# Performance work log

Measured on AMD Instinct MI355X. Metric: run time of the kernel, lower is better.

Reference implementation:

```python
import jax, jax.numpy as jnp
import numpy as np

B, C, H, W = 8, 256, 48, 48
EPS = 1e-5


def setup_inputs() -> dict:
    key = jax.random.key(0)
    ks = jax.random.split(key, 14)
    n = lambda k, shape, s=1.0: jax.random.normal(k, shape, dtype=jnp.float32) * s
    return {
        "fea_left": n(ks[0], (B, C, H, W)),
        "fea_right": n(ks[1], (B, C, H, W)),
        # query branch: conv1x1 weight (out,in), bias, BN gamma/beta/running_mean/running_var
        "Wq": n(ks[2], (C, C), 0.05), "bq": n(ks[3], (C,), 0.05),
        "gq": 1.0 + n(ks[4], (C,), 0.05), "betaq": n(ks[5], (C,), 0.05),
        "mq": n(ks[6], (C,), 0.05),
        "vq": jax.random.uniform(ks[7], (C,), dtype=jnp.float32, minval=0.5, maxval=1.5),
        # key branch
        "Wk": n(ks[8], (C, C), 0.05), "bk": n(ks[9], (C,), 0.05),
        "gk": 1.0 + n(ks[10], (C,), 0.05), "betak": n(ks[11], (C,), 0.05),
        "mk": n(ks[12], (C,), 0.05),
        "vk": jax.random.uniform(ks[13], (C,), dtype=jnp.float32, minval=0.5, maxval=1.5),
    }


def _proj(x, Wt, b, g, beta, m, v):
    # conv1x1 (bias=True) followed by eval-mode BatchNorm2d
    y = jnp.einsum("bchw,oc->bohw", x, Wt) + b[:, None, None]
    scale = g * jax.lax.rsqrt(v + EPS)
    return (y - m[:, None, None]) * scale[:, None, None] + beta[:, None, None]


def reference(fea_left, fea_right, Wq, bq, gq, betaq, mq, vq, Wk, bk, gk, betak, mk, vk):
    b, c, h, w = fea_left.shape

    def attend(qsrc, ksrc, vsrc):
        # torch .view(b,-1,c): raw row-major reinterpretation -> plain reshape
        Q = _proj(qsrc, Wq, bq, gq, betaq, mq, vq).reshape(b, -1, c)  # (b, h*w, c)
        K = _proj(ksrc, Wk, bk, gk, betak, mk, vk).reshape(b, -1, c)
        A = jax.nn.softmax(jnp.einsum("bnc,bmc->bnm", Q, K) / c, axis=-1)
        out = jnp.einsum("bnm,bmc->bnc", A, vsrc.reshape(b, -1, c))
        return out.transpose(0, 2, 1).reshape(b, c, h, w)

    cxr = attend(fea_left, fea_right, fea_right)
    enh = attend(fea_right, fea_left, fea_left)
    return (cxr, enh)
```

## Files before the change

kernel.cpp:

```cpp
#include <hip/hip_runtime.h>

#define CH    256
#define NTOK  2304
#define MATSZ (CH * NTOK)

typedef __bf16 bf16x8 __attribute__((ext_vector_type(8)));
typedef float  f4v    __attribute__((ext_vector_type(4)));
typedef float  f16v   __attribute__((ext_vector_type(16)));
typedef unsigned int u32x4 __attribute__((ext_vector_type(4)));

__device__ __forceinline__ unsigned short f2bf(float f) {
    union { float f; unsigned int i; } c;
    c.f = f;
    unsigned int x = c.i;
    x += 0x7fffu + ((x >> 16) & 1u);
    return (unsigned short)(x >> 16);
}

__device__ __forceinline__ bf16x8 cvt8(const float* p) {
    union { bf16x8 v; unsigned short s[8]; } u;
#pragma unroll
    for (int i = 0; i < 8; ++i) u.s[i] = f2bf(p[i]);
    return u.v;
}

__global__ __launch_bounds__(256) void tpose_k(
    const float* __restrict__ inL,
    const float* __restrict__ inR,
    unsigned short* __restrict__ out, int R, int Ccols)
{
    __shared__ unsigned short tile[64][72];
    int mat = blockIdx.y;
    const float* in = (mat >= 8 ? inR : inL) + (size_t)(mat & 7) * MATSZ;
    unsigned short* o = out + (size_t)mat * MATSZ;
    int tC = Ccols >> 6;
    int r0 = (blockIdx.x / tC) << 6;
    int c0 = (blockIdx.x % tC) << 6;
    int t = threadIdx.x;
    int col = t & 63, rs = t >> 6;
#pragma unroll
    for (int i = 0; i < 16; ++i) {
        int row = rs + i * 4;
        tile[row][col] = f2bf(in[(size_t)(r0 + row) * Ccols + c0 + col]);
    }
    __syncthreads();
#pragma unroll
    for (int i = 0; i < 16; ++i) {
        int crow = rs + i * 4;
        o[(size_t)(c0 + crow) * R + r0 + col] = tile[col][crow];
    }
}

__global__ __launch_bounds__(256, 2) void proj_k(
    const unsigned short* __restrict__ XT,
    const float* __restrict__ Wq_, const float* __restrict__ Wk_,
    const float* __restrict__ bq_, const float* __restrict__ bk_,
    const float* __restrict__ gq_, const float* __restrict__ gk_,
    const float* __restrict__ beq_, const float* __restrict__ bek_,
    const float* __restrict__ mq_, const float* __restrict__ mk_,
    const float* __restrict__ vq_, const float* __restrict__ vk_,
    unsigned short* __restrict__ Yout)
{
    __shared__ __align__(16) unsigned short Xs[64][264];
    int pb = blockIdx.y;
    int p = pb >> 3, b = pb & 7;
    int s = p & 1, br = p >> 1;
    const unsigned short* X = XT + (size_t)(s * 8 + b) * MATSZ;
    const float* W  = br ? Wk_ : Wq_;
    const float* bb = br ? bk_ : bq_;
    const float* gg = br ? gk_ : gq_;
    const float* be = br ? bek_ : beq_;
    const float* mm = br ? mk_ : mq_;
    const float* vv = br ? vk_ : vq_;
    unsigned short* Yo = Yout + (size_t)pb * MATSZ;

    int ot = blockIdx.x & 3, pt = blockIdx.x >> 2;
    int o0 = ot * 64, pos0 = pt * 64;
    int t = threadIdx.x;
    int w = t >> 6, lane = t & 63;
    int l15 = lane & 15, quad = lane >> 4;

    {
        int r = t >> 2, cq = (t & 3) << 6;
        const unsigned short* src = X + (size_t)(pos0 + r) * CH + cq;
        unsigned short* dst = &Xs[r][cq];
#pragma unroll
        for (int k = 0; k < 8; ++k)
            *(u32x4*)(dst + k * 8) = *(const u32x4*)(src + k * 8);
    }
    bf16x8 wf[8];
    {
        const float* wp = W + (size_t)(o0 + w * 16 + l15) * CH + quad * 8;
#pragma unroll
        for (int kc = 0; kc < 8; ++kc)
            wf[kc] = cvt8(wp + kc * 32);
    }
    __syncthreads();

    f4v zero4 = {0.f, 0.f, 0.f, 0.f};
    f4v acc[4] = {zero4, zero4, zero4, zero4};
#pragma unroll
    for (int kc = 0; kc < 8; ++kc) {
#pragma unroll
        for (int ct = 0; ct < 4; ++ct) {
            bf16x8 xb = *(const bf16x8*)(&Xs[ct * 16 + l15][kc * 32 + quad * 8]);
            acc[ct] = __builtin_amdgcn_mfma_f32_16x16x32_bf16(wf[kc], xb, acc[ct], 0, 0, 0);
        }
    }
#pragma unroll
    for (int r = 0; r < 4; ++r) {
        int o = o0 + w * 16 + quad * 4 + r;
        float scale = gg[o] * rsqrtf(vv[o] + 1e-5f);
        float shift = (bb[o] - mm[o]) * scale + be[o];
#pragma unroll
        for (int ct = 0; ct < 4; ++ct) {
            float val = acc[ct][r] * scale + shift;
            Yo[(size_t)o * NTOK + pos0 + ct * 16 + l15] = f2bf(val);
        }
    }
}

__global__ __launch_bounds__(256, 2) void attn_k(
    const unsigned short* __restrict__ Y,
    const unsigned short* __restrict__ VT,
    float* __restrict__ out)
{
    __shared__ __align__(16) unsigned char lds[74240];
    unsigned char* Ks = lds;
    unsigned char* Vs = lds + 32768;
    unsigned char* Pb = lds + 65536;
    float*         Ls = (float*)(lds + 73728);

    int bid = blockIdx.x;
    int wg = (bid & 7) * 72 + (bid >> 3);
    int qt = wg % 36;
    int ab = wg / 36;
    int a = ab >> 3, b = ab & 7;
    const unsigned short* Qp = Y + (size_t)(a * 8 + b) * MATSZ;
    const unsigned short* Kp = Y + (size_t)((3 - a) * 8 + b) * MATSZ;
    const unsigned short* Vp = VT + (size_t)((1 - a) * 8 + b) * MATSZ;
    float* Op = out + (size_t)ab * MATSZ;

    int t = threadIdx.x;
    int w = t >> 6, lane = t & 63;
    int l31 = lane & 31, h = lane >> 5;
    int qb = w >> 1;
    int kb = w & 1;
    int chh = w & 1;
    int rxor = (l31 & 7) << 4;

    const unsigned char* kS = (const unsigned char*)Kp
        + ((t * 16) ^ (((t >> 5) & 7) << 4));
    const unsigned char* vS = (const unsigned char*)Vp
        + (size_t)(t >> 3) * 4608
        + (((t & 7) * 16) ^ (((t >> 3) & 7) << 4));
    unsigned char* kD = Ks + t * 16;
    unsigned char* vD = Vs + t * 16;

    bf16x8 qf[16];
    {
        const unsigned short* qp = Qp + (size_t)(qt * 64 + qb * 32 + l31) * CH + h * 8;
#pragma unroll
        for (int ks = 0; ks < 16; ++ks)
            qf[ks] = *(const bf16x8*)(qp + ks * 16);
    }

    f16v acc_o[4];
#pragma unroll
    for (int c = 0; c < 4; ++c)
#pragma unroll
        for (int r = 0; r < 16; ++r) acc_o[c][r] = 0.f;
    float l_acc[16];
#pragma unroll
    for (int r = 0; r < 16; ++r) l_acc[r] = 0.f;

    for (int kt = 0; kt < 36; ++kt) {
        __syncthreads();
#pragma unroll
        for (int k = 0; k < 8; ++k)
            __builtin_amdgcn_global_load_lds(
                (const unsigned int*)(kS + (size_t)kt * 32768 + k * 4096),
                (unsigned int*)(kD + k * 4096), 16, 0, 0);
#pragma unroll
        for (int k = 0; k < 8; ++k)
            __builtin_amdgcn_global_load_lds(
                (const unsigned int*)(vS + (size_t)kt * 128 + (size_t)k * 147456),
                (unsigned int*)(vD + k * 4096), 16, 0, 0);
        __syncthreads();

        f16v accs;
#pragma unroll
        for (int r = 0; r < 16; ++r) accs[r] = 0.f;
        const unsigned char* krow = Ks + ((kb * 32 + l31) << 9);
#pragma unroll
        for (int ks = 0; ks < 16; ++ks) {
            bf16x8 kf = *(const bf16x8*)(krow + ((ks * 32 + h * 16) ^ rxor));
            accs = __builtin_amdgcn_mfma_f32_32x32x16_bf16(qf[ks], kf, accs, 0, 0, 0);
        }
#pragma unroll
        for (int r = 0; r < 16; ++r) {
            float pe = __expf(accs[r] * (1.0f / 256.0f));
            l_acc[r] += pe;
            int row = (r & 3) + 8 * (r >> 2) + 4 * h;
            int q = qb * 32 + row;
            *(__bf16*)(Pb + q * 128 + ((kb * 64 + l31 * 2) ^ ((row & 7) << 4))) = (__bf16)pe;
        }
        __syncthreads();

#pragma unroll
        for (int ks2 = 0; ks2 < 4; ++ks2) {
            bf16x8 pf = *(const bf16x8*)(Pb + ((qb * 32 + l31) << 7)
                                       + ((ks2 * 32 + h * 16) ^ rxor));
#pragma unroll
            for (int chb = 0; chb < 4; ++chb) {
                int ch = chh * 128 + chb * 32 + l31;
                bf16x8 vf = *(const bf16x8*)(Vs + (ch << 7)
                                           + ((ks2 * 32 + h * 16) ^ rxor));
                acc_o[chb] = __builtin_amdgcn_mfma_f32_32x32x16_bf16(pf, vf, acc_o[chb], 0, 0, 0);
            }
        }
    }

#pragma unroll
    for (int r = 0; r < 16; ++r) {
        float rs = l_acc[r];
        rs += __shfl_xor(rs, 1, 64);
        rs += __shfl_xor(rs, 2, 64);
        rs += __shfl_xor(rs, 4, 64);
        rs += __shfl_xor(rs, 8, 64);
        rs += __shfl_xor(rs, 16, 64);
        l_acc[r] = rs;
    }
    if (l31 == 0) {
#pragma unroll
        for (int r = 0; r < 16; ++r) {
            int row = (r & 3) + 8 * (r >> 2) + 4 * h;
            Ls[w * 32 + row] = l_acc[r];
        }
    }
    __syncthreads();
    float l_tot[16];
#pragma unroll
    for (int r = 0; r < 16; ++r) {
        int row = (r & 3) + 8 * (r >> 2) + 4 * h;
        l_tot[r] = Ls[w * 32 + row] + Ls[(w ^ 1) * 32 + row];
    }

    float* Ot = (float*)lds;
#pragma unroll
    for (int chb = 0; chb < 4; ++chb) {
        int c = chh * 128 + chb * 32 + l31;
        int cx = (c & 7) << 2;
#pragma unroll
        for (int rr = 0; rr < 4; ++rr) {
            f4v v4;
#pragma unroll
            for (int i = 0; i < 4; ++i)
                v4[i] = acc_o[chb][rr * 4 + i] / l_tot[rr * 4 + i];
            int q0 = qb * 32 + rr * 8 + h * 4;
            *(f4v*)(Ot + c * 64 + (q0 ^ cx)) = v4;
        }
    }
    __syncthreads();
#pragma unroll
    for (int p = 0; p < 16; ++p) {
        int c = p * 16 + (t >> 4);
        int q = (t & 15) * 4;
        f4v v4 = *(const f4v*)(Ot + c * 64 + (q ^ ((c & 7) << 2)));
        *(f4v*)(Op + (size_t)c * NTOK + qt * 64 + q) = v4;
    }
}

extern "C" void kernel_launch(void* const* d_in, const int* in_sizes, int n_in,
                              void* d_out, int out_size, void* d_ws, size_t ws_size,
                              hipStream_t stream) {
    (void)in_sizes; (void)n_in; (void)out_size; (void)ws_size;
    const float* feaL  = (const float*)d_in[0];
    const float* feaR  = (const float*)d_in[1];
    const float* Wq    = (const float*)d_in[2];
    const float* bq    = (const float*)d_in[3];
    const float* gq    = (const float*)d_in[4];
    const float* betaq = (const float*)d_in[5];
    const float* mq    = (const float*)d_in[6];
    const float* vq    = (const float*)d_in[7];
    const float* Wk    = (const float*)d_in[8];
    const float* bk    = (const float*)d_in[9];
    const float* gk    = (const float*)d_in[10];
    const float* betak = (const float*)d_in[11];
    const float* mk    = (const float*)d_in[12];
    const float* vk    = (const float*)d_in[13];

    unsigned short* XT = (unsigned short*)d_ws;
    unsigned short* VT = XT;
    unsigned short* Yb = XT + (size_t)16 * MATSZ;
    float* out = (float*)d_out;

    dim3 blk(256);
    tpose_k<<<dim3(144, 16), blk, 0, stream>>>(feaL, feaR, XT, 256, 2304);
    proj_k<<<dim3(144, 32), blk, 0, stream>>>(XT, Wq, Wk, bq, bk, gq, gk,
                                              betaq, betak, mq, mk, vq, vk, Yb);
    tpose_k<<<dim3(144, 16), blk, 0, stream>>>(feaL, feaR, VT, 2304, 256);
    attn_k<<<dim3(576), blk, 0, stream>>>(Yb, VT, out);
}
```

Before: 340.2 us.

## Prefetch next K/V tile into registers instead of direct global-to-LDS loads

Replaces the synchronous global_load_lds copies of K and V tiles with register prefetching: the next tile is loaded into registers while the current tile is being computed, then written to swizzled LDS after the barrier. The goal is to hide global memory latency behind the MFMA and softmax work. The cost is 64 extra VGPRs per thread, which may reduce occupancy, and an extra register-to-LDS store step.

```diff
diff --git a/kernel.cpp b/kernel.cpp
--- a/kernel.cpp
+++ b/kernel.cpp
@@ -149,13 +149,10 @@
     int chh = w & 1;
     int rxor = (l31 & 7) << 4;
 
-    const unsigned char* kS = (const unsigned char*)Kp
-        + ((t * 16) ^ (((t >> 5) & 7) << 4));
-    const unsigned char* vS = (const unsigned char*)Vp
-        + (size_t)(t >> 3) * 4608
-        + (((t & 7) * 16) ^ (((t >> 3) & 7) << 4));
-    unsigned char* kD = Ks + t * 16;
-    unsigned char* vD = Vs + t * 16;
+    const unsigned short* ksrc0 = Kp + t * 8;
+    const unsigned short* vsrc0 = Vp + (size_t)(t >> 3) * NTOK + ((t & 7) << 3);
+    char* kdst = (char*)Ks + ((t * 16) ^ (((t >> 5) & 7) << 4));
+    char* vdst = (char*)Vs + ((t * 16) ^ (((t >> 3) & 7) << 4));
 
     bf16x8 qf[16];
     {
@@ -174,19 +171,28 @@
 #pragma unroll
     for (int r = 0; r < 16; ++r) l_acc[r] = 0.f;
 
+    u32x4 kreg[8], vreg[8];
+#pragma unroll
+    for (int k = 0; k < 8; ++k) kreg[k] = *(const u32x4*)(ksrc0 + k * 2048);
+#pragma unroll
+    for (int k = 0; k < 8; ++k) vreg[k] = *(const u32x4*)(vsrc0 + (size_t)k * 32 * NTOK);
+
     for (int kt = 0; kt < 36; ++kt) {
         __syncthreads();
 #pragma unroll
-        for (int k = 0; k < 8; ++k)
-            __builtin_amdgcn_global_load_lds(
-                (const unsigned int*)(kS + (size_t)kt * 32768 + k * 4096),
-                (unsigned int*)(kD + k * 4096), 16, 0, 0);
-#pragma unroll
-        for (int k = 0; k < 8; ++k)
-            __builtin_amdgcn_global_load_lds(
-                (const unsigned int*)(vS + (size_t)kt * 128 + (size_t)k * 147456),
-                (unsigned int*)(vD + k * 4096), 16, 0, 0);
+        for (int k = 0; k < 8; ++k) *(u32x4*)(kdst + k * 4096) = kreg[k];
+#pragma unroll
+        for (int k = 0; k < 8; ++k) *(u32x4*)(vdst + k * 4096) = vreg[k];
         __syncthreads();
+
+        if (kt < 35) {
+            const unsigned short* kn = ksrc0 + (size_t)(kt + 1) * 16384;
+            const unsigned short* vn = vsrc0 + (size_t)(kt + 1) * 64;
+#pragma unroll
+            for (int k = 0; k < 8; ++k) kreg[k] = *(const u32x4*)(kn + k * 2048);
+#pragma unroll
+            for (int k = 0; k < 8; ++k) vreg[k] = *(const u32x4*)(vn + (size_t)k * 32 * NTOK);
+        }
 
         f16v accs;
 #pragma unroll
```

After: 411.1 us. 1.21x slower.

## Double-buffer K tiles in LDS and stream V directly into registers

Applied to the files above, without the earlier changes.

The attention loop now prefetches the next K tile into a second LDS buffer, reusing the region that used to hold V. V fragments are loaded straight from global memory into registers at the top of each iteration instead of being staged through LDS. The full __syncthreads calls are replaced with explicit s_waitcnt plus s_barrier so the in-flight prefetch does not block progress. Launch bounds are relaxed to one block per SM to leave room for the extra V registers. The trade-offs are redundant V global reads across waves, global-load latency exposed inside each iteration, and possibly lower occupancy.

```diff
diff --git a/kernel.cpp b/kernel.cpp
--- a/kernel.cpp
+++ b/kernel.cpp
@@ -120,14 +120,13 @@
     }
 }
 
-__global__ __launch_bounds__(256, 2) void attn_k(
+__global__ __launch_bounds__(256, 1) void attn_k(
     const unsigned short* __restrict__ Y,
     const unsigned short* __restrict__ VT,
     float* __restrict__ out)
 {
     __shared__ __align__(16) unsigned char lds[74240];
     unsigned char* Ks = lds;
-    unsigned char* Vs = lds + 32768;
     unsigned char* Pb = lds + 65536;
     float*         Ls = (float*)(lds + 73728);
 
@@ -151,11 +150,8 @@
 
     const unsigned char* kS = (const unsigned char*)Kp
         + ((t * 16) ^ (((t >> 5) & 7) << 4));
-    const unsigned char* vS = (const unsigned char*)Vp
-        + (size_t)(t >> 3) * 4608
-        + (((t & 7) * 16) ^ (((t >> 3) & 7) << 4));
     unsigned char* kD = Ks + t * 16;
-    unsigned char* vD = Vs + t * 16;
+    const unsigned short* VpT = Vp + (size_t)(chh * 128 + l31) * NTOK + h * 8;
 
     bf16x8 qf[16];
     {
@@ -174,24 +170,40 @@
 #pragma unroll
     for (int r = 0; r < 16; ++r) l_acc[r] = 0.f;
 
+#pragma unroll
+    for (int k = 0; k < 8; ++k)
+        __builtin_amdgcn_global_load_lds(
+            (const unsigned int*)(kS + k * 4096),
+            (unsigned int*)(kD + k * 4096), 16, 0, 0);
+
     for (int kt = 0; kt < 36; ++kt) {
-        __syncthreads();
-#pragma unroll
-        for (int k = 0; k < 8; ++k)
-            __builtin_amdgcn_global_load_lds(
-                (const unsigned int*)(kS + (size_t)kt * 32768 + k * 4096),
-                (unsigned int*)(kD + k * 4096), 16, 0, 0);
-#pragma unroll
-        for (int k = 0; k < 8; ++k)
-            __builtin_amdgcn_global_load_lds(
-                (const unsigned int*)(vS + (size_t)kt * 128 + (size_t)k * 147456),
-                (unsigned int*)(vD + k * 4096), 16, 0, 0);
-        __syncthreads();
+        bf16x8 vf[4][4];
+        {
+            const unsigned short* vp = VpT + kt * 64;
+#pragma unroll
+            for (int chb = 0; chb < 4; ++chb)
+#pragma unroll
+                for (int ks2 = 0; ks2 < 4; ++ks2)
+                    vf[chb][ks2] = *(const bf16x8*)(vp + (size_t)chb * 32 * NTOK + ks2 * 16);
+        }
+        {
+            int nt = kt + 1; if (nt == 36) nt = 0;
+            const unsigned char* ks_src = kS + (size_t)nt * 32768;
+            unsigned char* ks_dst = kD + ((kt + 1) & 1) * 32768;
+#pragma unroll
+            for (int k = 0; k < 8; ++k)
+                __builtin_amdgcn_global_load_lds(
+                    (const unsigned int*)(ks_src + k * 4096),
+                    (unsigned int*)(ks_dst + k * 4096), 16, 0, 0);
+        }
+        asm volatile("s_waitcnt vmcnt(24)" ::: "memory");
+        __builtin_amdgcn_s_barrier();
+        asm volatile("" ::: "memory");
 
         f16v accs;
 #pragma unroll
         for (int r = 0; r < 16; ++r) accs[r] = 0.f;
-        const unsigned char* krow = Ks + ((kb * 32 + l31) << 9);
+        const unsigned char* krow = Ks + (kt & 1) * 32768 + ((kb * 32 + l31) << 9);
 #pragma unroll
         for (int ks = 0; ks < 16; ++ks) {
             bf16x8 kf = *(const bf16x8*)(krow + ((ks * 32 + h * 16) ^ rxor));
@@ -205,19 +217,17 @@
             int q = qb * 32 + row;
             *(__bf16*)(Pb + q * 128 + ((kb * 64 + l31 * 2) ^ ((row & 7) << 4))) = (__bf16)pe;
         }
-        __syncthreads();
+        asm volatile("s_waitcnt lgkmcnt(0)" ::: "memory");
+        __builtin_amdgcn_s_barrier();
+        asm volatile("" ::: "memory");
 
 #pragma unroll
         for (int ks2 = 0; ks2 < 4; ++ks2) {
             bf16x8 pf = *(const bf16x8*)(Pb + ((qb * 32 + l31) << 7)
                                        + ((ks2 * 32 + h * 16) ^ rxor));
 #pragma unroll
-            for (int chb = 0; chb < 4; ++chb) {
-                int ch = chh * 128 + chb * 32 + l31;
-                bf16x8 vf = *(const bf16x8*)(Vs + (ch << 7)
-                                           + ((ks2 * 32 + h * 16) ^ rxor));
-                acc_o[chb] = __builtin_amdgcn_mfma_f32_32x32x16_bf16(pf, vf, acc_o[chb], 0, 0, 0);
-            }
+            for (int chb = 0; chb < 4; ++chb)
+                acc_o[chb] = __builtin_amdgcn_mfma_f32_32x32x16_bf16(pf, vf[chb][ks2], acc_o[chb], 0, 0, 0);
         }
     }
 
```

Measured after the change: 564.2 us. 1.66x slower.

## Prefetch next K/V tiles into LDS during compute with split barriers

Applied to the files above, without the earlier changes.

Restructures the attention key loop so the next K tile is loaded into LDS while the P·V MFMAs run, and the next V tile is loaded while the next Q·K phase runs. Full __syncthreads are replaced by raw s_barrier with explicit vmcnt waits, so the loop no longer stalls on both loads before computing. It keeps a single LDS buffer per operand, so correctness depends on the barrier and waitcnt placement. The vmcnt(8) count assumes a specific ordering of outstanding loads.

```diff
diff --git a/kernel.cpp b/kernel.cpp
--- a/kernel.cpp
+++ b/kernel.cpp
@@ -174,19 +174,22 @@
 #pragma unroll
     for (int r = 0; r < 16; ++r) l_acc[r] = 0.f;
 
+#pragma unroll
+    for (int k = 0; k < 8; ++k)
+        __builtin_amdgcn_global_load_lds(
+            (const unsigned int*)(kS + k * 4096),
+            (unsigned int*)(kD + k * 4096), 16, 0, 0);
+    asm volatile("" ::: "memory");
+#pragma unroll
+    for (int k = 0; k < 8; ++k)
+        __builtin_amdgcn_global_load_lds(
+            (const unsigned int*)(vS + (size_t)k * 147456),
+            (unsigned int*)(vD + k * 4096), 16, 0, 0);
+
     for (int kt = 0; kt < 36; ++kt) {
-        __syncthreads();
-#pragma unroll
-        for (int k = 0; k < 8; ++k)
-            __builtin_amdgcn_global_load_lds(
-                (const unsigned int*)(kS + (size_t)kt * 32768 + k * 4096),
-                (unsigned int*)(kD + k * 4096), 16, 0, 0);
-#pragma unroll
-        for (int k = 0; k < 8; ++k)
-            __builtin_amdgcn_global_load_lds(
-                (const unsigned int*)(vS + (size_t)kt * 128 + (size_t)k * 147456),
-                (unsigned int*)(vD + k * 4096), 16, 0, 0);
-        __syncthreads();
+        asm volatile("s_waitcnt vmcnt(8)" ::: "memory");
+        __builtin_amdgcn_s_barrier();
+        asm volatile("" ::: "memory");
 
         f16v accs;
 #pragma unroll
@@ -205,7 +208,19 @@
             int q = qb * 32 + row;
             *(__bf16*)(Pb + q * 128 + ((kb * 64 + l31 * 2) ^ ((row & 7) << 4))) = (__bf16)pe;
         }
-        __syncthreads();
+        asm volatile("s_waitcnt vmcnt(0) lgkmcnt(0)" ::: "memory");
+        __builtin_amdgcn_s_barrier();
+        asm volatile("" ::: "memory");
+
+        if (kt < 35) {
+            const unsigned char* ksn = kS + (size_t)(kt + 1) * 32768;
+#pragma unroll
+            for (int k = 0; k < 8; ++k)
+                __builtin_amdgcn_global_load_lds(
+                    (const unsigned int*)(ksn + k * 4096),
+                    (unsigned int*)(kD + k * 4096), 16, 0, 0);
+            asm volatile("" ::: "memory");
+        }
 
 #pragma unroll
         for (int ks2 = 0; ks2 < 4; ++ks2) {
@@ -218,6 +233,19 @@
                                            + ((ks2 * 32 + h * 16) ^ rxor));
                 acc_o[chb] = __builtin_amdgcn_mfma_f32_32x32x16_bf16(pf, vf, acc_o[chb], 0, 0, 0);
             }
+        }
+
+        __builtin_amdgcn_s_barrier();
+        asm volatile("" ::: "memory");
+
+        if (kt < 35) {
+            const unsigned char* vsn = vS + (size_t)(kt + 1) * 128;
+#pragma unroll
+            for (int k = 0; k < 8; ++k)
+                __builtin_amdgcn_global_load_lds(
+                    (const unsigned int*)(vsn + (size_t)k * 147456),
+                    (unsigned int*)(vD + k * 4096), 16, 0, 0);
+            asm volatile("" ::: "memory");
         }
     }
 
```

New measurement: 321.3 us. -5.5%, faster.
